# Performance work log

Hardware: AMD Instinct MI355X
Metric: run time of the kernel (lower is better)

Reference implementation:

```python
import jax, jax.numpy as jnp
import numpy as np

K = 3
NUM_STEP_COMBO = 5
BN_EPS = 1e-5


def setup_inputs() -> dict:
    key = jax.random.key(0)
    ks = jax.random.split(key, 10)
    N, E, D, H, O, G = 100000, 1600000, 48, 128, 12, 64
    x = jax.random.normal(ks[0], (N, D), dtype=jnp.float32)
    edge_index = jax.random.randint(ks[1], (2, E), 0, N, dtype=jnp.int64)
    batch = jnp.sort(jax.random.randint(ks[2], (N,), 0, G, dtype=jnp.int64))
    # ChebConv params: one [D, D] weight per Chebyshev order, shared bias
    W = jax.random.normal(ks[3], (K, D, D), dtype=jnp.float32) * 0.1
    b = jnp.zeros((D,), dtype=jnp.float32)
    gamma = jnp.ones((D,), dtype=jnp.float32)
    beta = jnp.zeros((D,), dtype=jnp.float32)
    W1 = jax.random.normal(ks[4], (D, H), dtype=jnp.float32) * 0.1
    b1 = jnp.zeros((H,), dtype=jnp.float32)
    W2 = jax.random.normal(ks[5], (H, O), dtype=jnp.float32) * 0.1
    b2 = jnp.zeros((O,), dtype=jnp.float32)
    return {"x": x, "edge_index": edge_index, "batch": batch, "num_graphs": 64,
            "W": W, "b": b, "gamma": gamma, "beta": beta,
            "W1": W1, "b1": b1, "W2": W2, "b2": b2}


def cheb_conv(x, row, col, W, b):
    # PyG ChebConv, sym norm, lambda_max=2 => L_hat = -D^{-1/2} A D^{-1/2}
    N = x.shape[0]
    deg = jax.ops.segment_sum(jnp.ones_like(row, dtype=x.dtype), row, num_segments=N)
    dinv = jnp.where(deg > 0, jax.lax.rsqrt(jnp.maximum(deg, 1.0)), 0.0)
    norm = (-dinv[row] * dinv[col])[:, None]  # [E,1] edge weights of L_hat

    def lhat(v):  # sparse matvec: gather neighbors, scale, scatter-add
        return jax.ops.segment_sum(norm * v[col], row, num_segments=N)

    Tx0 = x
    Tx1 = lhat(x)
    out = Tx0 @ W[0] + Tx1 @ W[1]
    Txkm2, Txkm1 = Tx0, Tx1
    for k in range(2, W.shape[0]):
        Txk = 2.0 * lhat(Txkm1) - Txkm2
        out = out + Txk @ W[k]
        Txkm2, Txkm1 = Txkm1, Txk
    return out + b


def reference(x, edge_index, batch, num_graphs, W, b, gamma, beta, W1, b1, W2, b2):
    row, col = edge_index[0], edge_index[1]
    N = x.shape[0]
    out = x
    for _ in range(NUM_STEP_COMBO):
        t = jax.nn.relu(cheb_conv(out, row, col, W, b))
        # BatchNorm1d (training-mode stats over all nodes, biased var)
        mean = jnp.mean(t, axis=0)
        var = jnp.mean((t - mean) ** 2, axis=0)
        t = gamma * (t - mean) * jax.lax.rsqrt(var + BN_EPS) + beta
        # graph_max_pool: per-node max over incoming neighbor features
        m = jax.ops.segment_max(t[col], row, num_segments=N)
        out = jnp.where(jnp.isneginf(m), 0.0, m)  # empty segments -> 0
    g = jax.ops.segment_sum(out, batch, num_segments=num_graphs)  # global_add_pool
    h = jax.nn.relu(g @ W1 + b1)
    return h @ W2 + b2
```

## Files before the change

### kernel.cpp

```cpp
#include <hip/hip_runtime.h>
#include <hip/hip_bf16.h>

#define D 48
#define GNUM 64
#define HDIM 128
#define ODIM 12
#define BN_EPS 1e-5f

typedef _Float16 half2v __attribute__((ext_vector_type(2)));
typedef _Float16 half4v __attribute__((ext_vector_type(4)));
typedef _Float16 half8v __attribute__((ext_vector_type(8)));

#if __has_builtin(__builtin_amdgcn_fdot2)
#define FDOT2(a, b, c) __builtin_amdgcn_fdot2((a), (b), (c), false)
#else
#define FDOT2(a, b, c) ((c) + (float)(a)[0] * (float)(b)[0] + (float)(a)[1] * (float)(b)[1])
#endif


__global__ __launch_bounds__(256) void k_deg(const int* __restrict__ row, int* __restrict__ deg, int E) {
    int e = blockIdx.x * 256 + threadIdx.x;
    if (e < E) atomicAdd(&deg[row[e]], 1);
}

__global__ __launch_bounds__(256) void k_dinv(const int* __restrict__ deg, float* __restrict__ dinv, int N) {
    int i = blockIdx.x * 256 + threadIdx.x;
    if (i < N) dinv[i] = deg[i] > 0 ? rsqrtf((float)deg[i]) : 0.f;
}

__global__ __launch_bounds__(256) void k_scan1(const int* __restrict__ deg, int* __restrict__ incl,
                                               int* __restrict__ bsum, int N) {
    __shared__ int s[256];
    int i = blockIdx.x * 256 + threadIdx.x;
    s[threadIdx.x] = (i < N) ? deg[i] : 0;
    __syncthreads();
    for (int off = 1; off < 256; off <<= 1) {
        int t = (threadIdx.x >= off) ? s[threadIdx.x - off] : 0;
        __syncthreads();
        s[threadIdx.x] += t;
        __syncthreads();
    }
    if (i < N) incl[i] = s[threadIdx.x];
    if (threadIdx.x == 255) bsum[blockIdx.x] = s[255];
}

__global__ __launch_bounds__(512) void k_scan2(int* __restrict__ bsum, int nb) {
    __shared__ int s[512];
    int t = threadIdx.x;
    s[t] = (t < nb) ? bsum[t] : 0;
    __syncthreads();
    for (int off = 1; off < 512; off <<= 1) {
        int v = (t >= off) ? s[t - off] : 0;
        __syncthreads();
        s[t] += v;
        __syncthreads();
    }
    if (t < nb) bsum[t] = s[t];
}

__global__ __launch_bounds__(256) void k_scan3(const int* __restrict__ incl, const int* __restrict__ bsum,
                                               int* __restrict__ rowptr, int N) {
    int i = blockIdx.x * 256 + threadIdx.x;
    if (i < N) {
        int add = (blockIdx.x > 0) ? bsum[blockIdx.x - 1] : 0;
        rowptr[i + 1] = incl[i] + add;
    }
    if (i == 0) rowptr[0] = 0;
}

__global__ __launch_bounds__(256) void k_fill(const int* __restrict__ row, const int* __restrict__ col,
                                              const int* __restrict__ rowptr, int* __restrict__ fillc,
                                              const float* __restrict__ dinv, int2* __restrict__ epair, int E) {
    int e = blockIdx.x * 256 + threadIdx.x;
    if (e < E) {
        int r = row[e], c = col[e];
        int p = rowptr[r] + atomicAdd(&fillc[r], 1);
        epair[p] = make_int2(c, __float_as_int(dinv[c]));
    }
}

__global__ __launch_bounds__(256) void k_cvt(const float* __restrict__ x, _Float16* __restrict__ xh, int n4) {
    int i = blockIdx.x * 256 + threadIdx.x;
    if (i < n4) {
        float4 v = ((const float4*)x)[i];
        half4v h;
        h.x = (_Float16)v.x; h.y = (_Float16)v.y; h.z = (_Float16)v.z; h.w = (_Float16)v.w;
        ((half4v*)xh)[i] = h;
    }
}


__global__ __launch_bounds__(256) void k_lhat(const _Float16* __restrict__ cur, const int* __restrict__ rowptr,
                                              const int2* __restrict__ epair, const float* __restrict__ dinv,
                                              _Float16* __restrict__ tx1, int N) {
    int lane = threadIdx.x & 63;
    int i = (blockIdx.x * 256 + threadIdx.x) >> 6;
    if (i >= N) return;
    int q = lane & 15, slot = lane >> 4;
    int qc = q < 12 ? q : 11;
    int s = rowptr[i], e = rowptr[i + 1];
    float a0 = 0.f, a1 = 0.f, a2 = 0.f, a3 = 0.f;
    int p = s + slot;
    for (; p + 4 < e; p += 8) {
        int2 ea = epair[p];
        int2 eb = epair[p + 4];
        float wa = __int_as_float(ea.y), wb = __int_as_float(eb.y);
        half4v ha = *(const half4v*)(cur + (size_t)ea.x * D + qc * 4);
        half4v hb = *(const half4v*)(cur + (size_t)eb.x * D + qc * 4);
        a0 += wa * (float)ha.x + wb * (float)hb.x;
        a1 += wa * (float)ha.y + wb * (float)hb.y;
        a2 += wa * (float)ha.z + wb * (float)hb.z;
        a3 += wa * (float)ha.w + wb * (float)hb.w;
    }
    if (p < e) {
        int2 ea = epair[p];
        float wa = __int_as_float(ea.y);
        half4v ha = *(const half4v*)(cur + (size_t)ea.x * D + qc * 4);
        a0 += wa * (float)ha.x; a1 += wa * (float)ha.y; a2 += wa * (float)ha.z; a3 += wa * (float)ha.w;
    }
    a0 += __shfl_xor(a0, 16); a1 += __shfl_xor(a1, 16); a2 += __shfl_xor(a2, 16); a3 += __shfl_xor(a3, 16);
    a0 += __shfl_xor(a0, 32); a1 += __shfl_xor(a1, 32); a2 += __shfl_xor(a2, 32); a3 += __shfl_xor(a3, 32);
    if (lane < 12) {
        float sc = -dinv[i];
        half4v o;
        o.x = (_Float16)(sc * a0); o.y = (_Float16)(sc * a1);
        o.z = (_Float16)(sc * a2); o.w = (_Float16)(sc * a3);
        *(half4v*)(tx1 + (size_t)i * D + lane * 4) = o;
    }
}

__global__ __launch_bounds__(256) void k_gather2(const _Float16* __restrict__ tx0, const _Float16* __restrict__ tx1,
                                                 const int* __restrict__ rowptr, const int2* __restrict__ epair,
                                                 const float* __restrict__ dinv, _Float16* __restrict__ tx2, int N) {
    int lane = threadIdx.x & 63;
    int i = (blockIdx.x * 256 + threadIdx.x) >> 6;
    if (i >= N) return;
    int q = lane & 15, slot = lane >> 4;
    int qc = q < 12 ? q : 11;
    int s = rowptr[i], e = rowptr[i + 1];
    float a0 = 0.f, a1 = 0.f, a2 = 0.f, a3 = 0.f;
    int p = s + slot;
    for (; p + 4 < e; p += 8) {
        int2 ea = epair[p];
        int2 eb = epair[p + 4];
        float wa = __int_as_float(ea.y), wb = __int_as_float(eb.y);
        half4v ha = *(const half4v*)(tx1 + (size_t)ea.x * D + qc * 4);
        half4v hb = *(const half4v*)(tx1 + (size_t)eb.x * D + qc * 4);
        a0 += wa * (float)ha.x + wb * (float)hb.x;
        a1 += wa * (float)ha.y + wb * (float)hb.y;
        a2 += wa * (float)ha.z + wb * (float)hb.z;
        a3 += wa * (float)ha.w + wb * (float)hb.w;
    }
    if (p < e) {
        int2 ea = epair[p];
        float wa = __int_as_float(ea.y);
        half4v ha = *(const half4v*)(tx1 + (size_t)ea.x * D + qc * 4);
        a0 += wa * (float)ha.x; a1 += wa * (float)ha.y; a2 += wa * (float)ha.z; a3 += wa * (float)ha.w;
    }
    a0 += __shfl_xor(a0, 16); a1 += __shfl_xor(a1, 16); a2 += __shfl_xor(a2, 16); a3 += __shfl_xor(a3, 16);
    a0 += __shfl_xor(a0, 32); a1 += __shfl_xor(a1, 32); a2 += __shfl_xor(a2, 32); a3 += __shfl_xor(a3, 32);
    if (lane < 12) {
        float sc = -2.f * dinv[i];
        half4v h0 = *(const half4v*)(tx0 + (size_t)i * D + lane * 4);
        half4v o;
        o.x = (_Float16)(sc * a0 - (float)h0.x); o.y = (_Float16)(sc * a1 - (float)h0.y);
        o.z = (_Float16)(sc * a2 - (float)h0.z); o.w = (_Float16)(sc * a3 - (float)h0.w);
        *(half4v*)(tx2 + (size_t)i * D + lane * 4) = o;
    }
}


__global__ __launch_bounds__(256) void k_dense(const _Float16* __restrict__ tx0, const _Float16* __restrict__ tx1,
                                               const _Float16* __restrict__ tx2, const float* __restrict__ W,
                                               const float* __restrict__ b, _Float16* __restrict__ tbuf, int N) {
    __shared__ half2v WH2[72 * D];
    __shared__ float bL[D];
    for (int t = threadIdx.x; t < 72 * D; t += 256) {
        int kp = t / D, j = t % D;
        half2v w;
        w.x = (_Float16)W[(2 * kp) * D + j];
        w.y = (_Float16)W[(2 * kp + 1) * D + j];
        WH2[t] = w;
    }
    if (threadIdx.x < D) bL[threadIdx.x] = b[threadIdx.x];
    __syncthreads();

    int base = (blockIdx.x * 256 + threadIdx.x) * 2;
    if (base >= N) return;
    bool two = (base + 1) < N;

    const _Float16* rowsA[3] = {tx0 + (size_t)base * D, tx1 + (size_t)base * D, tx2 + (size_t)base * D};
    size_t off2 = two ? D : 0;

    float acc0[D], acc1[D];
#pragma unroll
    for (int j = 0; j < D; ++j) { acc0[j] = bL[j]; acc1[j] = bL[j]; }

    for (int s = 0; s < 3; ++s) {
        const half2v* xa = (const half2v*)rowsA[s];
        const half2v* xb = (const half2v*)(rowsA[s] + off2);
#pragma unroll 4
        for (int g = 0; g < 24; ++g) {
            half2v va = xa[g], vb = xb[g];
            int kp = s * 24 + g;
            const half8v* wr = (const half8v*)&WH2[kp * D];
#pragma unroll
            for (int jc = 0; jc < 12; ++jc) {
                half8v w = wr[jc];
                half2v w0; w0.x = w[0]; w0.y = w[1];
                half2v w1; w1.x = w[2]; w1.y = w[3];
                half2v w2; w2.x = w[4]; w2.y = w[5];
                half2v w3; w3.x = w[6]; w3.y = w[7];
                acc0[jc * 4 + 0] = FDOT2(va, w0, acc0[jc * 4 + 0]);
                acc0[jc * 4 + 1] = FDOT2(va, w1, acc0[jc * 4 + 1]);
                acc0[jc * 4 + 2] = FDOT2(va, w2, acc0[jc * 4 + 2]);
                acc0[jc * 4 + 3] = FDOT2(va, w3, acc0[jc * 4 + 3]);
                acc1[jc * 4 + 0] = FDOT2(vb, w0, acc1[jc * 4 + 0]);
                acc1[jc * 4 + 1] = FDOT2(vb, w1, acc1[jc * 4 + 1]);
                acc1[jc * 4 + 2] = FDOT2(vb, w2, acc1[jc * 4 + 2]);
                acc1[jc * 4 + 3] = FDOT2(vb, w3, acc1[jc * 4 + 3]);
            }
        }
    }

    _Float16* o0 = tbuf + (size_t)base * D;
#pragma unroll
    for (int jc = 0; jc < 12; ++jc) {
        half4v h;
        h.x = (_Float16)fmaxf(acc0[jc * 4 + 0], 0.f);
        h.y = (_Float16)fmaxf(acc0[jc * 4 + 1], 0.f);
        h.z = (_Float16)fmaxf(acc0[jc * 4 + 2], 0.f);
        h.w = (_Float16)fmaxf(acc0[jc * 4 + 3], 0.f);
        *(half4v*)(o0 + jc * 4) = h;
    }
    if (two) {
        _Float16* o1 = o0 + D;
#pragma unroll
        for (int jc = 0; jc < 12; ++jc) {
            half4v h;
            h.x = (_Float16)fmaxf(acc1[jc * 4 + 0], 0.f);
            h.y = (_Float16)fmaxf(acc1[jc * 4 + 1], 0.f);
            h.z = (_Float16)fmaxf(acc1[jc * 4 + 2], 0.f);
            h.w = (_Float16)fmaxf(acc1[jc * 4 + 3], 0.f);
            *(half4v*)(o1 + jc * 4) = h;
        }
    }
}


__global__ __launch_bounds__(256) void k_bnstat(const _Float16* __restrict__ tbuf, float* __restrict__ bnstats, int N) {
    __shared__ float red[2 * D];
    if (threadIdx.x < 2 * D) red[threadIdx.x] = 0.f;
    __syncthreads();
    int tid = blockIdx.x * 256 + threadIdx.x;
    int q = tid % 12;
    int n0 = tid / 12;
    int stride = (gridDim.x * 256) / 12;
    float s0 = 0, s1 = 0, s2 = 0, s3 = 0, q0 = 0, q1 = 0, q2 = 0, q3 = 0;
    for (int n = n0; n < N; n += stride) {
        half4v h = *(const half4v*)(tbuf + (size_t)n * D + q * 4);
        float f0 = (float)h.x, f1 = (float)h.y, f2 = (float)h.z, f3 = (float)h.w;
        s0 += f0; s1 += f1; s2 += f2; s3 += f3;
        q0 += f0 * f0; q1 += f1 * f1; q2 += f2 * f2; q3 += f3 * f3;
    }
    atomicAdd(&red[q * 4 + 0], s0); atomicAdd(&red[q * 4 + 1], s1);
    atomicAdd(&red[q * 4 + 2], s2); atomicAdd(&red[q * 4 + 3], s3);
    atomicAdd(&red[D + q * 4 + 0], q0); atomicAdd(&red[D + q * 4 + 1], q1);
    atomicAdd(&red[D + q * 4 + 2], q2); atomicAdd(&red[D + q * 4 + 3], q3);
    __syncthreads();
    if (threadIdx.x < 2 * D) atomicAdd(&bnstats[threadIdx.x], red[threadIdx.x]);
}

__global__ __launch_bounds__(64) void k_bnfin(float* __restrict__ bnstats, const float* __restrict__ gamma,
                                              const float* __restrict__ beta, float* __restrict__ ss, float Ninv) {
    int t = threadIdx.x;
    if (t < D) {
        float mean = bnstats[t] * Ninv;
        float var = bnstats[D + t] * Ninv - mean * mean;
        var = fmaxf(var, 0.f);
        float sc = gamma[t] * rsqrtf(var + BN_EPS);
        ss[t] = sc;
        ss[D + t] = beta[t] - mean * sc;
        bnstats[t] = 0.f;
        bnstats[D + t] = 0.f;
    }
}


__global__ __launch_bounds__(256) void k_pool(const _Float16* __restrict__ tbuf, const int* __restrict__ rowptr,
                                              const int2* __restrict__ epair, const float* __restrict__ ss,
                                              _Float16* __restrict__ outh, int N) {
    int lane = threadIdx.x & 63;
    int i = (blockIdx.x * 256 + threadIdx.x) >> 6;
    if (i >= N) return;
    int q = lane & 15, slot = lane >> 4;
    int qc = q < 12 ? q : 11;
    int s = rowptr[i], e = rowptr[i + 1];
    float m0 = -3.4e38f, m1 = -3.4e38f, m2 = -3.4e38f, m3 = -3.4e38f;
    float n0 = 3.4e38f, n1 = 3.4e38f, n2 = 3.4e38f, n3 = 3.4e38f;
    int p = s + slot;
    for (; p + 4 < e; p += 8) {
        int ca = epair[p].x, cb = epair[p + 4].x;
        half4v ha = *(const half4v*)(tbuf + (size_t)ca * D + qc * 4);
        half4v hb = *(const half4v*)(tbuf + (size_t)cb * D + qc * 4);
        float a0 = (float)ha.x, a1 = (float)ha.y, a2 = (float)ha.z, a3 = (float)ha.w;
        float b0 = (float)hb.x, b1 = (float)hb.y, b2 = (float)hb.z, b3 = (float)hb.w;
        m0 = fmaxf(m0, fmaxf(a0, b0)); m1 = fmaxf(m1, fmaxf(a1, b1));
        m2 = fmaxf(m2, fmaxf(a2, b2)); m3 = fmaxf(m3, fmaxf(a3, b3));
        n0 = fminf(n0, fminf(a0, b0)); n1 = fminf(n1, fminf(a1, b1));
        n2 = fminf(n2, fminf(a2, b2)); n3 = fminf(n3, fminf(a3, b3));
    }
    if (p < e) {
        int ca = epair[p].x;
        half4v ha = *(const half4v*)(tbuf + (size_t)ca * D + qc * 4);
        float a0 = (float)ha.x, a1 = (float)ha.y, a2 = (float)ha.z, a3 = (float)ha.w;
        m0 = fmaxf(m0, a0); m1 = fmaxf(m1, a1); m2 = fmaxf(m2, a2); m3 = fmaxf(m3, a3);
        n0 = fminf(n0, a0); n1 = fminf(n1, a1); n2 = fminf(n2, a2); n3 = fminf(n3, a3);
    }
    m0 = fmaxf(m0, __shfl_xor(m0, 16)); m1 = fmaxf(m1, __shfl_xor(m1, 16));
    m2 = fmaxf(m2, __shfl_xor(m2, 16)); m3 = fmaxf(m3, __shfl_xor(m3, 16));
    m0 = fmaxf(m0, __shfl_xor(m0, 32)); m1 = fmaxf(m1, __shfl_xor(m1, 32));
    m2 = fmaxf(m2, __shfl_xor(m2, 32)); m3 = fmaxf(m3, __shfl_xor(m3, 32));
    n0 = fminf(n0, __shfl_xor(n0, 16)); n1 = fminf(n1, __shfl_xor(n1, 16));
    n2 = fminf(n2, __shfl_xor(n2, 16)); n3 = fminf(n3, __shfl_xor(n3, 16));
    n0 = fminf(n0, __shfl_xor(n0, 32)); n1 = fminf(n1, __shfl_xor(n1, 32));
    n2 = fminf(n2, __shfl_xor(n2, 32)); n3 = fminf(n3, __shfl_xor(n3, 32));
    if (lane < 12) {
        float4 sc = *(const float4*)(ss + lane * 4);
        float4 sh = *(const float4*)(ss + D + lane * 4);
        half4v o;
        if (s == e) {
            o.x = (_Float16)0.f; o.y = (_Float16)0.f; o.z = (_Float16)0.f; o.w = (_Float16)0.f;
        } else {
            float v0 = (sc.x >= 0.f) ? sc.x * m0 + sh.x : sc.x * n0 + sh.x;
            float v1 = (sc.y >= 0.f) ? sc.y * m1 + sh.y : sc.y * n1 + sh.y;
            float v2 = (sc.z >= 0.f) ? sc.z * m2 + sh.z : sc.z * n2 + sh.z;
            float v3 = (sc.w >= 0.f) ? sc.w * m3 + sh.w : sc.w * n3 + sh.w;
            o.x = (_Float16)v0; o.y = (_Float16)v1; o.z = (_Float16)v2; o.w = (_Float16)v3;
        }
        *(half4v*)(outh + (size_t)i * D + lane * 4) = o;
    }
}


__global__ __launch_bounds__(256) void k_gpool(const _Float16* __restrict__ outh, const int* __restrict__ batch,
                                               float* __restrict__ g, int N, int chunk) {
    int lane = threadIdx.x & 63;
    int wid = (blockIdx.x * 256 + threadIdx.x) >> 6;
    int start = wid * chunk;
    if (start >= N || lane >= 12) return;
    int end = start + chunk;
    if (end > N) end = N;
    int curb = batch[start];
    float a0 = 0.f, a1 = 0.f, a2 = 0.f, a3 = 0.f;
    for (int i = start; i < end; ++i) {
        int bi = batch[i];
        if (bi != curb) {
            atomicAdd(&g[curb * D + lane * 4 + 0], a0); atomicAdd(&g[curb * D + lane * 4 + 1], a1);
            atomicAdd(&g[curb * D + lane * 4 + 2], a2); atomicAdd(&g[curb * D + lane * 4 + 3], a3);
            curb = bi; a0 = a1 = a2 = a3 = 0.f;
        }
        half4v h = *(const half4v*)(outh + (size_t)i * D + lane * 4);
        a0 += (float)h.x; a1 += (float)h.y; a2 += (float)h.z; a3 += (float)h.w;
    }
    atomicAdd(&g[curb * D + lane * 4 + 0], a0); atomicAdd(&g[curb * D + lane * 4 + 1], a1);
    atomicAdd(&g[curb * D + lane * 4 + 2], a2); atomicAdd(&g[curb * D + lane * 4 + 3], a3);
}

__global__ __launch_bounds__(256) void k_mlp(const float* __restrict__ g, const float* __restrict__ W1,
                                             const float* __restrict__ b1, const float* __restrict__ W2,
                                             const float* __restrict__ b2, float* __restrict__ out) {
    __shared__ float gL[GNUM * D];
    __shared__ float hL[GNUM * HDIM];
    __shared__ float W1L[D * HDIM];
    int t = threadIdx.x;
    for (int i = t; i < GNUM * D; i += 256) gL[i] = g[i];
    for (int i = t; i < D * HDIM; i += 256) W1L[i] = W1[i];
    __syncthreads();
    for (int i = t; i < GNUM * HDIM; i += 256) {
        int gi = i >> 7, hj = i & 127;
        float a = b1[hj];
        for (int k = 0; k < D; ++k) a += gL[gi * D + k] * W1L[k * HDIM + hj];
        hL[i] = fmaxf(a, 0.f);
    }
    __syncthreads();
    for (int i = t; i < GNUM * ODIM; i += 256) {
        int gi = i / ODIM, oj = i % ODIM;
        float a = b2[oj];
        for (int k = 0; k < HDIM; ++k) a += hL[gi * HDIM + k] * W2[k * ODIM + oj];
        out[i] = a;
    }
}


extern "C" void kernel_launch(void* const* d_in, const int* in_sizes, int n_in,
                              void* d_out, int out_size, void* d_ws, size_t ws_size,
                              hipStream_t stream) {
    const float* x     = (const float*)d_in[0];
    const int*   ei    = (const int*)d_in[1];
    const int*   batch = (const int*)d_in[2];
    const float* W     = (const float*)d_in[4];
    const float* b     = (const float*)d_in[5];
    const float* gamma = (const float*)d_in[6];
    const float* beta  = (const float*)d_in[7];
    const float* W1    = (const float*)d_in[8];
    const float* b1    = (const float*)d_in[9];
    const float* W2    = (const float*)d_in[10];
    const float* b2    = (const float*)d_in[11];

    int N = in_sizes[0] / D;
    int E = in_sizes[1] / 2;
    const int* row = ei;
    const int* col = ei + E;

    char* w = (char*)d_ws;
    auto alloc = [&](size_t bytes) { char* p = w; w += (bytes + 255) & ~(size_t)255; return p; };
    int*       deg     = (int*)alloc((size_t)N * 4);
    float*     dinv    = (float*)alloc((size_t)N * 4);
    int*       fillc   = (int*)alloc((size_t)N * 4);
    int*       incl    = (int*)alloc((size_t)N * 4);
    int*       bsum    = (int*)alloc(4096);
    int*       rowptr  = (int*)alloc((size_t)(N + 1) * 4);
    int2*      epair   = (int2*)alloc((size_t)E * 8);
    _Float16*  xh      = (_Float16*)alloc((size_t)N * D * 2 + 64);
    _Float16*  tx1h    = (_Float16*)alloc((size_t)N * D * 2 + 64);
    _Float16*  tx2h    = (_Float16*)alloc((size_t)N * D * 2 + 64);
    _Float16*  tbufh   = (_Float16*)alloc((size_t)N * D * 2 + 64);
    _Float16*  outh    = (_Float16*)alloc((size_t)N * D * 2 + 64);
    float*     bnstats = (float*)alloc(2 * D * 4);
    float*     ss      = (float*)alloc(2 * D * 4);
    float*     g       = (float*)alloc((size_t)GNUM * D * 4);

    hipMemsetAsync(deg, 0, (size_t)N * 4, stream);
    hipMemsetAsync(fillc, 0, (size_t)N * 4, stream);
    hipMemsetAsync(bnstats, 0, 2 * D * 4, stream);
    hipMemsetAsync(g, 0, (size_t)GNUM * D * 4, stream);

    int nbE = (E + 255) / 256;
    int nbN = (N + 255) / 256;

    k_deg<<<nbE, 256, 0, stream>>>(row, deg, E);
    k_dinv<<<nbN, 256, 0, stream>>>(deg, dinv, N);
    k_scan1<<<nbN, 256, 0, stream>>>(deg, incl, bsum, N);
    k_scan2<<<1, 512, 0, stream>>>(bsum, nbN);
    k_scan3<<<nbN, 256, 0, stream>>>(incl, bsum, rowptr, N);
    k_fill<<<nbE, 256, 0, stream>>>(row, col, rowptr, fillc, dinv, epair, E);
    int n4 = N * D / 4;
    k_cvt<<<(n4 + 255) / 256, 256, 0, stream>>>(x, xh, n4);

    int nbWave = (N * 64 + 255) / 256;
    int nbDense = ((N + 1) / 2 + 255) / 256;
    const _Float16* cur = xh;
    for (int step = 0; step < 5; ++step) {
        k_lhat<<<nbWave, 256, 0, stream>>>(cur, rowptr, epair, dinv, tx1h, N);
        k_gather2<<<nbWave, 256, 0, stream>>>(cur, tx1h, rowptr, epair, dinv, tx2h, N);
        k_dense<<<nbDense, 256, 0, stream>>>(cur, tx1h, tx2h, W, b, tbufh, N);
        k_bnstat<<<120, 256, 0, stream>>>(tbufh, bnstats, N);
        k_bnfin<<<1, 64, 0, stream>>>(bnstats, gamma, beta, ss, 1.f / (float)N);
        k_pool<<<nbWave, 256, 0, stream>>>(tbufh, rowptr, epair, ss, outh, N);
        cur = outh;
    }

    int chunk = 32;
    int nwaves = (N + chunk - 1) / chunk;
    int nbG = (nwaves * 64 + 255) / 256;
    k_gpool<<<nbG, 256, 0, stream>>>(outh, batch, g, N, chunk);
    k_mlp<<<1, 256, 0, stream>>>(g, W1, b1, W2, b2, (float*)d_out);
}
```

Measured before the change: 1.281 ms.

## Use MFMA for dense Chebyshev transform, fuse BN stats, unroll gathers

The per-node FDOT2 dense kernel is replaced by a wave-level 16x16x16 f16 MFMA kernel over 16-node tiles, with weights transposed into LDS. The BN sum and sum-of-squares are now accumulated in the dense kernel's epilogue, and the finalize step is folded into the pool kernel, which removes two launches and a full re-read of the activations per step. Per-step stat buffers replace the reset logic. The gather loops in lhat, gather2 and pool are unrolled to four edges per lane to keep more loads in flight. Costs: scattered 2-byte output stores in the dense epilogue, and every pool block recomputes the BN scale and shift.

```diff
diff --git a/kernel.cpp b/kernel.cpp
--- a/kernel.cpp
+++ b/kernel.cpp
@@ -7,15 +7,10 @@
 #define ODIM 12
 #define BN_EPS 1e-5f
 
-typedef _Float16 half2v __attribute__((ext_vector_type(2)));
 typedef _Float16 half4v __attribute__((ext_vector_type(4)));
-typedef _Float16 half8v __attribute__((ext_vector_type(8)));
-
-#if __has_builtin(__builtin_amdgcn_fdot2)
-#define FDOT2(a, b, c) __builtin_amdgcn_fdot2((a), (b), (c), false)
-#else
-#define FDOT2(a, b, c) ((c) + (float)(a)[0] * (float)(b)[0] + (float)(a)[1] * (float)(b)[1])
-#endif
+typedef float f32x4 __attribute__((ext_vector_type(4)));
+
+#define MFMA16(a, b, c) __builtin_amdgcn_mfma_f32_16x16x16f16((a), (b), (c), 0, 0, 0)
 
 
 __global__ __launch_bounds__(256) void k_deg(const int* __restrict__ row, int* __restrict__ deg, int E) {
@@ -101,18 +96,20 @@
     int s = rowptr[i], e = rowptr[i + 1];
     float a0 = 0.f, a1 = 0.f, a2 = 0.f, a3 = 0.f;
     int p = s + slot;
-    for (; p + 4 < e; p += 8) {
-        int2 ea = epair[p];
-        int2 eb = epair[p + 4];
-        float wa = __int_as_float(ea.y), wb = __int_as_float(eb.y);
-        half4v ha = *(const half4v*)(cur + (size_t)ea.x * D + qc * 4);
-        half4v hb = *(const half4v*)(cur + (size_t)eb.x * D + qc * 4);
-        a0 += wa * (float)ha.x + wb * (float)hb.x;
-        a1 += wa * (float)ha.y + wb * (float)hb.y;
-        a2 += wa * (float)ha.z + wb * (float)hb.z;
-        a3 += wa * (float)ha.w + wb * (float)hb.w;
-    }
-    if (p < e) {
+    for (; p + 12 < e; p += 16) {
+        int2 e0 = epair[p], e1 = epair[p + 4], e2 = epair[p + 8], e3 = epair[p + 12];
+        half4v h0 = *(const half4v*)(cur + (size_t)e0.x * D + qc * 4);
+        half4v h1 = *(const half4v*)(cur + (size_t)e1.x * D + qc * 4);
+        half4v h2 = *(const half4v*)(cur + (size_t)e2.x * D + qc * 4);
+        half4v h3 = *(const half4v*)(cur + (size_t)e3.x * D + qc * 4);
+        float w0 = __int_as_float(e0.y), w1 = __int_as_float(e1.y);
+        float w2 = __int_as_float(e2.y), w3 = __int_as_float(e3.y);
+        a0 += w0 * (float)h0.x + w1 * (float)h1.x + w2 * (float)h2.x + w3 * (float)h3.x;
+        a1 += w0 * (float)h0.y + w1 * (float)h1.y + w2 * (float)h2.y + w3 * (float)h3.y;
+        a2 += w0 * (float)h0.z + w1 * (float)h1.z + w2 * (float)h2.z + w3 * (float)h3.z;
+        a3 += w0 * (float)h0.w + w1 * (float)h1.w + w2 * (float)h2.w + w3 * (float)h3.w;
+    }
+    for (; p < e; p += 4) {
         int2 ea = epair[p];
         float wa = __int_as_float(ea.y);
         half4v ha = *(const half4v*)(cur + (size_t)ea.x * D + qc * 4);
@@ -140,18 +137,20 @@
     int s = rowptr[i], e = rowptr[i + 1];
     float a0 = 0.f, a1 = 0.f, a2 = 0.f, a3 = 0.f;
     int p = s + slot;
-    for (; p + 4 < e; p += 8) {
-        int2 ea = epair[p];
-        int2 eb = epair[p + 4];
-        float wa = __int_as_float(ea.y), wb = __int_as_float(eb.y);
-        half4v ha = *(const half4v*)(tx1 + (size_t)ea.x * D + qc * 4);
-        half4v hb = *(const half4v*)(tx1 + (size_t)eb.x * D + qc * 4);
-        a0 += wa * (float)ha.x + wb * (float)hb.x;
-        a1 += wa * (float)ha.y + wb * (float)hb.y;
-        a2 += wa * (float)ha.z + wb * (float)hb.z;
-        a3 += wa * (float)ha.w + wb * (float)hb.w;
-    }
-    if (p < e) {
+    for (; p + 12 < e; p += 16) {
+        int2 e0 = epair[p], e1 = epair[p + 4], e2 = epair[p + 8], e3 = epair[p + 12];
+        half4v h0 = *(const half4v*)(tx1 + (size_t)e0.x * D + qc * 4);
+        half4v h1 = *(const half4v*)(tx1 + (size_t)e1.x * D + qc * 4);
+        half4v h2 = *(const half4v*)(tx1 + (size_t)e2.x * D + qc * 4);
+        half4v h3 = *(const half4v*)(tx1 + (size_t)e3.x * D + qc * 4);
+        float w0 = __int_as_float(e0.y), w1 = __int_as_float(e1.y);
+        float w2 = __int_as_float(e2.y), w3 = __int_as_float(e3.y);
+        a0 += w0 * (float)h0.x + w1 * (float)h1.x + w2 * (float)h2.x + w3 * (float)h3.x;
+        a1 += w0 * (float)h0.y + w1 * (float)h1.y + w2 * (float)h2.y + w3 * (float)h3.y;
+        a2 += w0 * (float)h0.z + w1 * (float)h1.z + w2 * (float)h2.z + w3 * (float)h3.z;
+        a3 += w0 * (float)h0.w + w1 * (float)h1.w + w2 * (float)h2.w + w3 * (float)h3.w;
+    }
+    for (; p < e; p += 4) {
         int2 ea = epair[p];
         float wa = __int_as_float(ea.y);
         half4v ha = *(const half4v*)(tx1 + (size_t)ea.x * D + qc * 4);
@@ -172,126 +171,96 @@
 
 __global__ __launch_bounds__(256) void k_dense(const _Float16* __restrict__ tx0, const _Float16* __restrict__ tx1,
                                                const _Float16* __restrict__ tx2, const float* __restrict__ W,
-                                               const float* __restrict__ b, _Float16* __restrict__ tbuf, int N) {
-    __shared__ half2v WH2[72 * D];
+                                               const float* __restrict__ b, _Float16* __restrict__ tbuf,
+                                               float* __restrict__ bnst, int N) {
+    __shared__ _Float16 WT[48][152];
     __shared__ float bL[D];
-    for (int t = threadIdx.x; t < 72 * D; t += 256) {
-        int kp = t / D, j = t % D;
-        half2v w;
-        w.x = (_Float16)W[(2 * kp) * D + j];
-        w.y = (_Float16)W[(2 * kp + 1) * D + j];
-        WH2[t] = w;
-    }
-    if (threadIdx.x < D) bL[threadIdx.x] = b[threadIdx.x];
-    __syncthreads();
-
-    int base = (blockIdx.x * 256 + threadIdx.x) * 2;
-    if (base >= N) return;
-    bool two = (base + 1) < N;
-
-    const _Float16* rowsA[3] = {tx0 + (size_t)base * D, tx1 + (size_t)base * D, tx2 + (size_t)base * D};
-    size_t off2 = two ? D : 0;
-
-    float acc0[D], acc1[D];
+    __shared__ float bns[2 * D];
+    int t = threadIdx.x;
+    for (int idx = t; idx < 144 * D; idx += 256) {
+        int k = idx / D, c = idx % D;
+        WT[c][k] = (_Float16)W[idx];
+    }
+    if (t < D) bL[t] = b[t];
+    if (t < 2 * D) bns[t] = 0.f;
+    __syncthreads();
+
+    int lane = t & 63, wave = t >> 6;
+    int node0 = (blockIdx.x * 4 + wave) * 16;
+    if (node0 < N) {
+        int col = lane & 15, kg = lane >> 4;
+        int nodeA = node0 + col;
+        bool inA = nodeA < N;
+        const _Float16* __restrict__ Xs0 = tx0 + (size_t)nodeA * D;
+        const _Float16* __restrict__ Xs1 = tx1 + (size_t)nodeA * D;
+        const _Float16* __restrict__ Xs2 = tx2 + (size_t)nodeA * D;
+        const _Float16* __restrict__ Xs[3] = {Xs0, Xs1, Xs2};
+        f32x4 acc0 = {}, acc1 = {}, acc2 = {};
 #pragma unroll
-    for (int j = 0; j < D; ++j) { acc0[j] = bL[j]; acc1[j] = bL[j]; }
-
-    for (int s = 0; s < 3; ++s) {
-        const half2v* xa = (const half2v*)rowsA[s];
-        const half2v* xb = (const half2v*)(rowsA[s] + off2);
-#pragma unroll 4
-        for (int g = 0; g < 24; ++g) {
-            half2v va = xa[g], vb = xb[g];
-            int kp = s * 24 + g;
-            const half8v* wr = (const half8v*)&WH2[kp * D];
+        for (int s = 0; s < 3; ++s) {
 #pragma unroll
-            for (int jc = 0; jc < 12; ++jc) {
-                half8v w = wr[jc];
-                half2v w0; w0.x = w[0]; w0.y = w[1];
-                half2v w1; w1.x = w[2]; w1.y = w[3];
-                half2v w2; w2.x = w[4]; w2.y = w[5];
-                half2v w3; w3.x = w[6]; w3.y = w[7];
-                acc0[jc * 4 + 0] = FDOT2(va, w0, acc0[jc * 4 + 0]);
-                acc0[jc * 4 + 1] = FDOT2(va, w1, acc0[jc * 4 + 1]);
-                acc0[jc * 4 + 2] = FDOT2(va, w2, acc0[jc * 4 + 2]);
-                acc0[jc * 4 + 3] = FDOT2(va, w3, acc0[jc * 4 + 3]);
-                acc1[jc * 4 + 0] = FDOT2(vb, w0, acc1[jc * 4 + 0]);
-                acc1[jc * 4 + 1] = FDOT2(vb, w1, acc1[jc * 4 + 1]);
-                acc1[jc * 4 + 2] = FDOT2(vb, w2, acc1[jc * 4 + 2]);
-                acc1[jc * 4 + 3] = FDOT2(vb, w3, acc1[jc * 4 + 3]);
+            for (int kb = 0; kb < 48; kb += 16) {
+                half4v a = {};
+                if (inA) a = *(const half4v*)(Xs[s] + kb + kg * 4);
+                int kk = s * 48 + kb + kg * 4;
+                half4v b0 = *(const half4v*)&WT[col][kk];
+                half4v b1 = *(const half4v*)&WT[16 + col][kk];
+                half4v b2 = *(const half4v*)&WT[32 + col][kk];
+                acc0 = MFMA16(a, b0, acc0);
+                acc1 = MFMA16(a, b1, acc1);
+                acc2 = MFMA16(a, b2, acc2);
             }
         }
-    }
-
-    _Float16* o0 = tbuf + (size_t)base * D;
+        float s0 = 0.f, q0 = 0.f, s1 = 0.f, q1 = 0.f, s2 = 0.f, q2 = 0.f;
 #pragma unroll
-    for (int jc = 0; jc < 12; ++jc) {
-        half4v h;
-        h.x = (_Float16)fmaxf(acc0[jc * 4 + 0], 0.f);
-        h.y = (_Float16)fmaxf(acc0[jc * 4 + 1], 0.f);
-        h.z = (_Float16)fmaxf(acc0[jc * 4 + 2], 0.f);
-        h.w = (_Float16)fmaxf(acc0[jc * 4 + 3], 0.f);
-        *(half4v*)(o0 + jc * 4) = h;
-    }
-    if (two) {
-        _Float16* o1 = o0 + D;
-#pragma unroll
-        for (int jc = 0; jc < 12; ++jc) {
-            half4v h;
-            h.x = (_Float16)fmaxf(acc1[jc * 4 + 0], 0.f);
-            h.y = (_Float16)fmaxf(acc1[jc * 4 + 1], 0.f);
-            h.z = (_Float16)fmaxf(acc1[jc * 4 + 2], 0.f);
-            h.w = (_Float16)fmaxf(acc1[jc * 4 + 3], 0.f);
-            *(half4v*)(o1 + jc * 4) = h;
+        for (int i = 0; i < 4; ++i) {
+            int nd = node0 + kg * 4 + i;
+            float v0 = fmaxf(acc0[i] + bL[col], 0.f);
+            float v1 = fmaxf(acc1[i] + bL[16 + col], 0.f);
+            float v2 = fmaxf(acc2[i] + bL[32 + col], 0.f);
+            if (nd < N) {
+                _Float16* o = tbuf + (size_t)nd * D;
+                o[col] = (_Float16)v0;
+                o[16 + col] = (_Float16)v1;
+                o[32 + col] = (_Float16)v2;
+                s0 += v0; q0 += v0 * v0;
+                s1 += v1; q1 += v1 * v1;
+                s2 += v2; q2 += v2 * v2;
+            }
         }
-    }
-}
-
-
-__global__ __launch_bounds__(256) void k_bnstat(const _Float16* __restrict__ tbuf, float* __restrict__ bnstats, int N) {
-    __shared__ float red[2 * D];
-    if (threadIdx.x < 2 * D) red[threadIdx.x] = 0.f;
-    __syncthreads();
-    int tid = blockIdx.x * 256 + threadIdx.x;
-    int q = tid % 12;
-    int n0 = tid / 12;
-    int stride = (gridDim.x * 256) / 12;
-    float s0 = 0, s1 = 0, s2 = 0, s3 = 0, q0 = 0, q1 = 0, q2 = 0, q3 = 0;
-    for (int n = n0; n < N; n += stride) {
-        half4v h = *(const half4v*)(tbuf + (size_t)n * D + q * 4);
-        float f0 = (float)h.x, f1 = (float)h.y, f2 = (float)h.z, f3 = (float)h.w;
-        s0 += f0; s1 += f1; s2 += f2; s3 += f3;
-        q0 += f0 * f0; q1 += f1 * f1; q2 += f2 * f2; q3 += f3 * f3;
-    }
-    atomicAdd(&red[q * 4 + 0], s0); atomicAdd(&red[q * 4 + 1], s1);
-    atomicAdd(&red[q * 4 + 2], s2); atomicAdd(&red[q * 4 + 3], s3);
-    atomicAdd(&red[D + q * 4 + 0], q0); atomicAdd(&red[D + q * 4 + 1], q1);
-    atomicAdd(&red[D + q * 4 + 2], q2); atomicAdd(&red[D + q * 4 + 3], q3);
-    __syncthreads();
-    if (threadIdx.x < 2 * D) atomicAdd(&bnstats[threadIdx.x], red[threadIdx.x]);
-}
-
-__global__ __launch_bounds__(64) void k_bnfin(float* __restrict__ bnstats, const float* __restrict__ gamma,
-                                              const float* __restrict__ beta, float* __restrict__ ss, float Ninv) {
+        s0 += __shfl_xor(s0, 16); s0 += __shfl_xor(s0, 32);
+        q0 += __shfl_xor(q0, 16); q0 += __shfl_xor(q0, 32);
+        s1 += __shfl_xor(s1, 16); s1 += __shfl_xor(s1, 32);
+        q1 += __shfl_xor(q1, 16); q1 += __shfl_xor(q1, 32);
+        s2 += __shfl_xor(s2, 16); s2 += __shfl_xor(s2, 32);
+        q2 += __shfl_xor(q2, 16); q2 += __shfl_xor(q2, 32);
+        if (lane < 16) {
+            atomicAdd(&bns[col], s0);      atomicAdd(&bns[D + col], q0);
+            atomicAdd(&bns[16 + col], s1); atomicAdd(&bns[D + 16 + col], q1);
+            atomicAdd(&bns[32 + col], s2); atomicAdd(&bns[D + 32 + col], q2);
+        }
+    }
+    __syncthreads();
+    if (t < 2 * D) atomicAdd(&bnst[t], bns[t]);
+}
+
+
+__global__ __launch_bounds__(256) void k_pool(const _Float16* __restrict__ tbuf, const int* __restrict__ rowptr,
+                                              const int2* __restrict__ epair, const float* __restrict__ bnst,
+                                              const float* __restrict__ gamma, const float* __restrict__ beta,
+                                              float Ninv, _Float16* __restrict__ outh, int N) {
+    __shared__ float ssL[2 * D];
     int t = threadIdx.x;
     if (t < D) {
-        float mean = bnstats[t] * Ninv;
-        float var = bnstats[D + t] * Ninv - mean * mean;
-        var = fmaxf(var, 0.f);
+        float mean = bnst[t] * Ninv;
+        float var = fmaxf(bnst[D + t] * Ninv - mean * mean, 0.f);
         float sc = gamma[t] * rsqrtf(var + BN_EPS);
-        ss[t] = sc;
-        ss[D + t] = beta[t] - mean * sc;
-        bnstats[t] = 0.f;
-        bnstats[D + t] = 0.f;
-    }
-}
-
-
-__global__ __launch_bounds__(256) void k_pool(const _Float16* __restrict__ tbuf, const int* __restrict__ rowptr,
-                                              const int2* __restrict__ epair, const float* __restrict__ ss,
-                                              _Float16* __restrict__ outh, int N) {
-    int lane = threadIdx.x & 63;
-    int i = (blockIdx.x * 256 + threadIdx.x) >> 6;
+        ssL[t] = sc;
+        ssL[D + t] = beta[t] - mean * sc;
+    }
+    __syncthreads();
+    int lane = t & 63;
+    int i = (blockIdx.x * 256 + t) >> 6;
     if (i >= N) return;
     int q = lane & 15, slot = lane >> 4;
     int qc = q < 12 ? q : 11;
@@ -299,18 +268,26 @@
     float m0 = -3.4e38f, m1 = -3.4e38f, m2 = -3.4e38f, m3 = -3.4e38f;
     float n0 = 3.4e38f, n1 = 3.4e38f, n2 = 3.4e38f, n3 = 3.4e38f;
     int p = s + slot;
-    for (; p + 4 < e; p += 8) {
-        int ca = epair[p].x, cb = epair[p + 4].x;
-        half4v ha = *(const half4v*)(tbuf + (size_t)ca * D + qc * 4);
-        half4v hb = *(const half4v*)(tbuf + (size_t)cb * D + qc * 4);
-        float a0 = (float)ha.x, a1 = (float)ha.y, a2 = (float)ha.z, a3 = (float)ha.w;
-        float b0 = (float)hb.x, b1 = (float)hb.y, b2 = (float)hb.z, b3 = (float)hb.w;
-        m0 = fmaxf(m0, fmaxf(a0, b0)); m1 = fmaxf(m1, fmaxf(a1, b1));
-        m2 = fmaxf(m2, fmaxf(a2, b2)); m3 = fmaxf(m3, fmaxf(a3, b3));
-        n0 = fminf(n0, fminf(a0, b0)); n1 = fminf(n1, fminf(a1, b1));
-        n2 = fminf(n2, fminf(a2, b2)); n3 = fminf(n3, fminf(a3, b3));
-    }
-    if (p < e) {
+    for (; p + 12 < e; p += 16) {
+        int c0 = epair[p].x, c1 = epair[p + 4].x, c2 = epair[p + 8].x, c3 = epair[p + 12].x;
+        half4v h0 = *(const half4v*)(tbuf + (size_t)c0 * D + qc * 4);
+        half4v h1 = *(const half4v*)(tbuf + (size_t)c1 * D + qc * 4);
+        half4v h2 = *(const half4v*)(tbuf + (size_t)c2 * D + qc * 4);
+        half4v h3 = *(const half4v*)(tbuf + (size_t)c3 * D + qc * 4);
+        float x00 = (float)h0.x, x01 = (float)h0.y, x02 = (float)h0.z, x03 = (float)h0.w;
+        float x10 = (float)h1.x, x11 = (float)h1.y, x12 = (float)h1.z, x13 = (float)h1.w;
+        float x20 = (float)h2.x, x21 = (float)h2.y, x22 = (float)h2.z, x23 = (float)h2.w;
+        float x30 = (float)h3.x, x31 = (float)h3.y, x32 = (float)h3.z, x33 = (float)h3.w;
+        m0 = fmaxf(m0, fmaxf(fmaxf(x00, x10), fmaxf(x20, x30)));
+        m1 = fmaxf(m1, fmaxf(fmaxf(x01, x11), fmaxf(x21, x31)));
+        m2 = fmaxf(m2, fmaxf(fmaxf(x02, x12), fmaxf(x22, x32)));
+        m3 = fmaxf(m3, fmaxf(fmaxf(x03, x13), fmaxf(x23, x33)));
+        n0 = fminf(n0, fminf(fminf(x00, x10), fminf(x20, x30)));
+        n1 = fminf(n1, fminf(fminf(x01, x11), fminf(x21, x31)));
+        n2 = fminf(n2, fminf(fminf(x02, x12), fminf(x22, x32)));
+        n3 = fminf(n3, fminf(fminf(x03, x13), fminf(x23, x33)));
+    }
+    for (; p < e; p += 4) {
         int ca = epair[p].x;
         half4v ha = *(const half4v*)(tbuf + (size_t)ca * D + qc * 4);
         float a0 = (float)ha.x, a1 = (float)ha.y, a2 = (float)ha.z, a3 = (float)ha.w;
@@ -326,8 +303,8 @@
     n0 = fminf(n0, __shfl_xor(n0, 32)); n1 = fminf(n1, __shfl_xor(n1, 32));
     n2 = fminf(n2, __shfl_xor(n2, 32)); n3 = fminf(n3, __shfl_xor(n3, 32));
     if (lane < 12) {
-        float4 sc = *(const float4*)(ss + lane * 4);
-        float4 sh = *(const float4*)(ss + D + lane * 4);
+        float4 sc = *(const float4*)(ssL + lane * 4);
+        float4 sh = *(const float4*)(ssL + D + lane * 4);
         half4v o;
         if (s == e) {
             o.x = (_Float16)0.f; o.y = (_Float16)0.f; o.z = (_Float16)0.f; o.w = (_Float16)0.f;
@@ -427,14 +404,13 @@
     _Float16*  tx2h    = (_Float16*)alloc((size_t)N * D * 2 + 64);
     _Float16*  tbufh   = (_Float16*)alloc((size_t)N * D * 2 + 64);
     _Float16*  outh    = (_Float16*)alloc((size_t)N * D * 2 + 64);
-    float*     bnstats = (float*)alloc(2 * D * 4);
-    float*     ss      = (float*)alloc(2 * D * 4);
+    float*     bnstats = (float*)alloc(5 * 2 * D * 4);
     float*     g       = (float*)alloc((size_t)GNUM * D * 4);
 
-    hipMemsetAsync(deg, 0, (size_t)N * 4, stream);
-    hipMemsetAsync(fillc, 0, (size_t)N * 4, stream);
-    hipMemsetAsync(bnstats, 0, 2 * D * 4, stream);
-    hipMemsetAsync(g, 0, (size_t)GNUM * D * 4, stream);
+    (void)hipMemsetAsync(deg, 0, (size_t)N * 4, stream);
+    (void)hipMemsetAsync(fillc, 0, (size_t)N * 4, stream);
+    (void)hipMemsetAsync(bnstats, 0, 5 * 2 * D * 4, stream);
+    (void)hipMemsetAsync(g, 0, (size_t)GNUM * D * 4, stream);
 
     int nbE = (E + 255) / 256;
     int nbN = (N + 255) / 256;
@@ -449,15 +425,15 @@
     k_cvt<<<(n4 + 255) / 256, 256, 0, stream>>>(x, xh, n4);
 
     int nbWave = (N * 64 + 255) / 256;
-    int nbDense = ((N + 1) / 2 + 255) / 256;
+    int nbDense = (((N + 15) / 16) + 3) / 4;
+    float Ninv = 1.f / (float)N;
     const _Float16* cur = xh;
     for (int step = 0; step < 5; ++step) {
+        float* bnst = bnstats + step * 2 * D;
         k_lhat<<<nbWave, 256, 0, stream>>>(cur, rowptr, epair, dinv, tx1h, N);
         k_gather2<<<nbWave, 256, 0, stream>>>(cur, tx1h, rowptr, epair, dinv, tx2h, N);
-        k_dense<<<nbDense, 256, 0, stream>>>(cur, tx1h, tx2h, W, b, tbufh, N);
-        k_bnstat<<<120, 256, 0, stream>>>(tbufh, bnstats, N);
-        k_bnfin<<<1, 64, 0, stream>>>(bnstats, gamma, beta, ss, 1.f / (float)N);
-        k_pool<<<nbWave, 256, 0, stream>>>(tbufh, rowptr, epair, ss, outh, N);
+        k_dense<<<nbDense, 256, 0, stream>>>(cur, tx1h, tx2h, W, b, tbufh, bnst, N);
+        k_pool<<<nbWave, 256, 0, stream>>>(tbufh, rowptr, epair, bnst, gamma, beta, Ninv, outh, N);
         cur = outh;
     }
 
```

New measurement: 1.302 ms. Within noise of the previous version (+1.6%).
